# Optimization experiments

Measured on AMD Instinct MI355X. Metric: run time of the kernel, lower is better.

Reference implementation:

```python
import jax, jax.numpy as jnp
import numpy as np

N, C, OUT, S, NS = 8192, 256, 256, 8, 16  # points, in_planes, out_planes, share_planes, nsample
MID = OUT  # mid_planes = out_planes // 1
H = OUT // S  # linear_w bottleneck width
EPS = 1e-5


def _bn(x, g, b, m, v):
    # inference-mode BatchNorm1d over last (channel) dim
    return (x - m) * jax.lax.rsqrt(v + EPS) * g + b


def _knn_idx(p, k):
    # squared euclidean distances, (N,N); indices of k nearest (self included)
    sq = jnp.sum(p * p, axis=1)
    d = sq[:, None] + sq[None, :] - 2.0 * (p @ p.T)
    return jax.lax.top_k(-jax.lax.stop_gradient(d), k)[1]  # (N, k) int32


def setup_inputs() -> dict:
    key = jax.random.key(0)
    ks = jax.random.split(key, 24)
    g = lambda i, shape, s=0.05: jax.random.normal(ks[i], shape, jnp.float32) * s
    u = lambda i, shape: jax.random.uniform(ks[i], shape, dtype=jnp.float32)
    return {
        'p': u(0, (N, 3)),
        'x': g(1, (N, C), 1.0),
        'w_q': g(2, (C, MID)), 'b_q': jnp.zeros((MID,), jnp.float32),
        'w_k': g(3, (C, MID)), 'b_k': jnp.zeros((MID,), jnp.float32),
        'w_v': g(4, (C, OUT)), 'b_v': jnp.zeros((OUT,), jnp.float32),
        'p_w1': g(5, (3, 3), 0.5), 'p_b1': jnp.zeros((3,), jnp.float32),
        'p_bn_g': u(6, (3,)) + 0.5, 'p_bn_b': g(7, (3,), 0.1),
        'p_bn_m': g(8, (3,), 0.1), 'p_bn_v': u(9, (3,)) + 0.5,
        'p_w2': g(10, (3, OUT), 0.5), 'p_b2': jnp.zeros((OUT,), jnp.float32),
        'w_bn1_g': u(11, (MID,)) + 0.5, 'w_bn1_b': g(12, (MID,), 0.1),
        'w_bn1_m': g(13, (MID,), 0.1), 'w_bn1_v': u(14, (MID,)) + 0.5,
        'w_l1_w': g(15, (MID, H)), 'w_l1_b': jnp.zeros((H,), jnp.float32),
        'w_bn2_g': u(16, (H,)) + 0.5, 'w_bn2_b': g(17, (H,), 0.1),
        'w_bn2_m': g(18, (H,), 0.1), 'w_bn2_v': u(19, (H,)) + 0.5,
        'w_l2_w': g(20, (H, H)), 'w_l2_b': jnp.zeros((H,), jnp.float32),
    }


def reference(p, x, w_q, b_q, w_k, b_k, w_v, b_v,
              p_w1, p_b1, p_bn_g, p_bn_b, p_bn_m, p_bn_v, p_w2, p_b2,
              w_bn1_g, w_bn1_b, w_bn1_m, w_bn1_v, w_l1_w, w_l1_b,
              w_bn2_g, w_bn2_b, w_bn2_m, w_bn2_v, w_l2_w, w_l2_b):
    # PointTransformerLayer forward (single point cloud, o = [N])
    xq = x @ w_q + b_q            # (N, MID)
    xk = x @ w_k + b_k            # (N, MID)
    xv = x @ w_v + b_v            # (N, OUT)

    idx = _knn_idx(p, NS)         # (N, NS) KNN neighbor indices
    pr_xyz = p[idx] - p[:, None, :]   # (N, NS, 3) relative coords (with_xyz=True)
    xk_g = xk[idx]                # (N, NS, MID) gathered keys
    xv_g = xv[idx]                # (N, NS, OUT) gathered values

    # linear_p: Linear(3,3) -> BN -> ReLU -> Linear(3, OUT)
    pr = jax.nn.relu(_bn(pr_xyz @ p_w1 + p_b1, p_bn_g, p_bn_b, p_bn_m, p_bn_v))
    pr = pr @ p_w2 + p_b2         # (N, NS, OUT)

    # einops reduce 'n ns (i j)->n ns j' with j=MID is identity since MID==OUT
    r_qk = xk_g - xq[:, None, :] + pr   # (N, NS, MID)

    # linear_w: BN -> ReLU -> Linear(MID,H) -> BN -> ReLU -> Linear(H,H)
    w = jax.nn.relu(_bn(r_qk, w_bn1_g, w_bn1_b, w_bn1_m, w_bn1_v)) @ w_l1_w + w_l1_b
    w = jax.nn.relu(_bn(w, w_bn2_g, w_bn2_b, w_bn2_m, w_bn2_v)) @ w_l2_w + w_l2_b
    w = jax.nn.softmax(w, axis=1)       # softmax over neighbors (dim=1)

    v = (xv_g + pr).reshape(N, NS, S, H)      # 'n ns (s i) -> n ns s i'
    out = jnp.einsum('ntsi,nti->nsi', v, w)   # weighted aggregation over neighbors
    return out.reshape(N, OUT)
```

## Files before the change

### kernel.cpp

```cpp
#include <hip/hip_runtime.h>
#include <hip/hip_bf16.h>
#include <math.h>

#define N_PTS 8192
#define C_IN  256
#define OUT_C 256
#define NSAMP 16
#define H_W   32
#define EPSBN 1e-5f
#define GDIM  8
#define NCELL (GDIM * GDIM * GDIM)
#define CAPC  768

typedef short bf16x8 __attribute__((ext_vector_type(8)));
typedef float f32x4  __attribute__((ext_vector_type(4)));

__device__ __forceinline__ float dist2(const float4 a, const float4 b) {
  float dot = a.x * b.x + a.y * b.y + a.z * b.z;
  return a.w + b.w - 2.0f * dot;
}

__device__ __forceinline__ unsigned long long make_key(float d, int j) {
  unsigned int di = __float_as_uint(d);
  unsigned int ord = ((int)di >= 0) ? (di ^ 0x80000000u) : ~di;
  return ((unsigned long long)ord << 32) | (unsigned int)j;
}

__device__ __forceinline__ void chain_insert(unsigned long long (&ak)[16], unsigned long long key) {
  if (key < ak[0]) {
    #pragma unroll
    for (int s = 0; s < 15; ++s) {
      unsigned long long mn = ak[s] < key ? ak[s] : key;
      unsigned long long nx = ak[s + 1];
      ak[s] = nx > mn ? nx : mn;
    }
    ak[15] = ak[15] < key ? ak[15] : key;
  }
}

__device__ __forceinline__ void merge16(unsigned long long (&A)[16], int m) {
  unsigned long long B[16], t[16];
  #pragma unroll
  for (int s = 0; s < 16; ++s) B[s] = __shfl_xor(A[s], m, 64);
  #pragma unroll
  for (int s = 0; s < 16; ++s) t[s] = A[s] < B[15 - s] ? A[s] : B[15 - s];
  #pragma unroll
  for (int k = 8; k >= 1; k >>= 1) {
    #pragma unroll
    for (int s = 0; s < 16; ++s) {
      if (!(s & k)) {
        unsigned long long lo = t[s] < t[s | k] ? t[s] : t[s | k];
        unsigned long long hi = t[s] < t[s | k] ? t[s | k] : t[s];
        t[s] = lo; t[s | k] = hi;
      }
    }
  }
  #pragma unroll
  for (int s = 0; s < 16; ++s) A[s] = t[s];
}

__global__ __launch_bounds__(256) void prep_kernel(
    const float* __restrict__ p, const float* __restrict__ x,
    const float* __restrict__ wq, const float* __restrict__ wk, const float* __restrict__ wv,
    const float* __restrict__ bq, const float* __restrict__ bk, const float* __restrict__ bv,
    const float* __restrict__ l1w, const float* __restrict__ l2w,
    float4* __restrict__ p4, __hip_bfloat16* __restrict__ Bp, float* __restrict__ biasp,
    __hip_bfloat16* __restrict__ x_bf,
    __hip_bfloat16* __restrict__ l1wp, __hip_bfloat16* __restrict__ l2wp,
    int* __restrict__ hist, int* __restrict__ pt_cell) {
  int tid = blockIdx.x * blockDim.x + threadIdx.x;
  if (tid < 48 * 32 * 16 * 8) {
    int kj = tid & 7, n = (tid >> 3) & 15, kb = (tid >> 7) & 31, nt = tid >> 12;
    int k = kb * 8 + kj, col = nt * 16 + n;
    float v;
    if (col < 256)      v = wq[k * 256 + col];
    else if (col < 512) v = wk[k * 256 + (col - 256)];
    else                v = wv[k * 256 + (col - 512)];
    Bp[tid] = __float2bfloat16(v);
  }
  if (tid < 768) {
    biasp[tid] = tid < 256 ? bq[tid] : (tid < 512 ? bk[tid - 256] : bv[tid - 512]);
  }
  if (tid < 8192) {
    int kj = tid & 7, n = (tid >> 3) & 15, kb = (tid >> 7) & 31, nt = (tid >> 12) & 1;
    int k = kb * 8 + kj, col = nt * 16 + n;
    l1wp[tid] = __float2bfloat16(l1w[k * 32 + col]);
  }
  if (tid < 1024) {
    int kj = tid & 7, n = (tid >> 3) & 15, kb = (tid >> 7) & 3, nt = (tid >> 9) & 1;
    int k = kb * 8 + kj, col = nt * 16 + n;
    l2wp[tid] = __float2bfloat16(l2w[k * 32 + col]);
  }
  if (tid < N_PTS) {
    float px = p[tid * 3 + 0], py = p[tid * 3 + 1], pz = p[tid * 3 + 2];
    float sq = px * px;
    sq += py * py;
    sq += pz * pz;
    p4[tid] = make_float4(px, py, pz, sq);
    int cx = min(GDIM - 1, max(0, (int)(px * GDIM)));
    int cy = min(GDIM - 1, max(0, (int)(py * GDIM)));
    int cz = min(GDIM - 1, max(0, (int)(pz * GDIM)));
    int cell = (cz * GDIM + cy) * GDIM + cx;
    pt_cell[tid] = cell;
    atomicAdd(&hist[cell], 1);
  }
  if (tid < N_PTS * C_IN) x_bf[tid] = __float2bfloat16(x[tid]);
}

__global__ __launch_bounds__(512) void scan512(const int* __restrict__ hist, int* __restrict__ cell_start) {
  __shared__ int buf[NCELL];
  int t = threadIdx.x;
  buf[t] = hist[t];
  __syncthreads();
  for (int off = 1; off < NCELL; off <<= 1) {
    int add = (t >= off) ? buf[t - off] : 0;
    __syncthreads();
    buf[t] += add;
    __syncthreads();
  }
  cell_start[t + 1] = buf[t];
  if (t == 0) cell_start[0] = 0;
}

__global__ __launch_bounds__(256) void scatter_kernel(
    const float4* __restrict__ p4, const int* __restrict__ pt_cell,
    const int* __restrict__ cell_start, int* __restrict__ cursor,
    float4* __restrict__ sp4, int* __restrict__ sidx, int* __restrict__ rank) {
  int tid = blockIdx.x * blockDim.x + threadIdx.x;
  if (tid < N_PTS) {
    int c = pt_cell[tid];
    int pos = cell_start[c] + atomicAdd(&cursor[c], 1);
    sp4[pos] = p4[tid];
    sidx[pos] = tid;
    rank[tid] = pos;
  }
}

__global__ __launch_bounds__(256) void knn_grid(
    const float4* __restrict__ sp4, const int* __restrict__ sidx,
    const int* __restrict__ cell_start, int* __restrict__ nbr) {
  __shared__ float4 cpos[CAPC];
  __shared__ int    cidx[CAPC];
  __shared__ int cell_s0_s[27];
  __shared__ int pref_s[28];
  __shared__ int nc_s, total_s;

  const int cell = blockIdx.x;
  const int tid = threadIdx.x;
  const int hcx = cell & 7, hcy = (cell >> 3) & 7, hcz = cell >> 6;
  const int cs = cell_start[cell], ce = cell_start[cell + 1];

  const int ax0 = max(hcx - 1, 0), ax1 = min(hcx + 1, GDIM - 1);
  const int ay0 = max(hcy - 1, 0), ay1 = min(hcy + 1, GDIM - 1);
  const int az0 = max(hcz - 1, 0), az1 = min(hcz + 1, GDIM - 1);

  if (tid == 0) {
    int off = 0, m = 0;
    for (int cz = az0; cz <= az1; ++cz)
      for (int cy = ay0; cy <= ay1; ++cy)
        for (int cx = ax0; cx <= ax1; ++cx) {
          int cc = (cz * GDIM + cy) * GDIM + cx;
          cell_s0_s[m] = cell_start[cc];
          pref_s[m] = off;
          off += cell_start[cc + 1] - cell_start[cc];
          ++m;
        }
    pref_s[m] = off;
    nc_s = m;
    total_s = off;
  }
  __syncthreads();
  const int nc = nc_s, total = total_s;

  for (int idx = tid; idx < total && idx < CAPC; idx += 256) {
    int c = 0;
    while (c + 1 < nc && pref_s[c + 1] <= idx) ++c;
    int g = cell_s0_s[c] + (idx - pref_s[c]);
    cpos[idx] = sp4[g];
    cidx[idx] = sidx[g];
  }
  __syncthreads();

  const int ptl = tid >> 4, slice = tid & 15;

  for (int p0 = cs; p0 < ce; p0 += 16) {
    const int np = min(16, ce - p0);
    const bool pok = ptl < np;
    const int ld = pok ? (p0 + ptl) : cs;
    const float4 pi = sp4[ld];
    const int orig = sidx[ld];

    unsigned long long ak[16];
    #pragma unroll
    for (int s = 0; s < 16; ++s) ak[s] = ~0ULL;

    for (int idx = slice; idx < total; idx += 16) {
      float4 q;
      int qi;
      if (idx < CAPC) { q = cpos[idx]; qi = cidx[idx]; }
      else {
        int c = 0;
        while (c + 1 < nc && pref_s[c + 1] <= idx) ++c;
        int g = cell_s0_s[c] + (idx - pref_s[c]);
        q = sp4[g]; qi = sidx[g];
      }
      chain_insert(ak, make_key(dist2(pi, q), qi));
    }

    unsigned long long asc[16];
    #pragma unroll
    for (int s = 0; s < 16; ++s) asc[s] = ak[15 - s];
    merge16(asc, 1);
    merge16(asc, 2);
    merge16(asc, 4);
    merge16(asc, 8);

    if (slice == 0 && pok) {
      unsigned long long akm[16];
      #pragma unroll
      for (int s = 0; s < 16; ++s) akm[s] = asc[15 - s];
      float r;
      if (akm[0] == ~0ULL) {
        r = 1e9f;
      } else {
        unsigned int ord = (unsigned int)(akm[0] >> 32);
        unsigned int di = (ord & 0x80000000u) ? (ord ^ 0x80000000u) : ~ord;
        float d16 = __uint_as_float(di);
        r = sqrtf(fmaxf(d16, 0.f)) * 1.001f + 1e-4f;
      }
      int lx = (int)fminf(fmaxf(floorf((pi.x - r) * GDIM), 0.f), (float)(GDIM - 1));
      int ux = (int)fminf(fmaxf(floorf((pi.x + r) * GDIM), 0.f), (float)(GDIM - 1));
      int ly = (int)fminf(fmaxf(floorf((pi.y - r) * GDIM), 0.f), (float)(GDIM - 1));
      int uy = (int)fminf(fmaxf(floorf((pi.y + r) * GDIM), 0.f), (float)(GDIM - 1));
      int lz = (int)fminf(fmaxf(floorf((pi.z - r) * GDIM), 0.f), (float)(GDIM - 1));
      int uz = (int)fminf(fmaxf(floorf((pi.z + r) * GDIM), 0.f), (float)(GDIM - 1));
      if (lx < ax0 || ux > ax1 || ly < ay0 || uy > ay1 || lz < az0 || uz > az1) {
        for (int cz = lz; cz <= uz; ++cz)
          for (int cy = ly; cy <= uy; ++cy)
            for (int cx = lx; cx <= ux; ++cx) {
              if (cx >= ax0 && cx <= ax1 && cy >= ay0 && cy <= ay1 && cz >= az0 && cz <= az1)
                continue;
              int cc = (cz * GDIM + cy) * GDIM + cx;
              int s0 = cell_start[cc], e0 = cell_start[cc + 1];
              for (int k = s0; k < e0; ++k) {
                float4 q = sp4[k];
                chain_insert(akm, make_key(dist2(pi, q), sidx[k]));
              }
            }
      }
      #pragma unroll
      for (int s = 0; s < 16; ++s) nbr[orig * NSAMP + s] = (int)(akm[s] & 0xFFFFFFFFu);
    }
  }
}

__global__ __launch_bounds__(256) void gemm_qkv_mfma(
    const __hip_bfloat16* __restrict__ x_bf, const __hip_bfloat16* __restrict__ Bp,
    const float* __restrict__ biasp, const int* __restrict__ rank,
    __hip_bfloat16* __restrict__ xqkv) {
  const int w = threadIdx.x >> 6;
  const int lane = threadIdx.x & 63;
  const int gw = blockIdx.x * 4 + w;
  const int m0 = (gw & 127) * 64;
  const int nt4 = (gw >> 7) * 4;
  const int n = lane & 15, q = lane >> 4;

  f32x4 acc[4][4];
  #pragma unroll
  for (int mi = 0; mi < 4; ++mi)
    #pragma unroll
    for (int ni = 0; ni < 4; ++ni) acc[mi][ni] = (f32x4){0.f, 0.f, 0.f, 0.f};

  for (int k0 = 0; k0 < 256; k0 += 32) {
    bf16x8 af[4], bfr[4];
    #pragma unroll
    for (int mi = 0; mi < 4; ++mi)
      af[mi] = *(const bf16x8*)&x_bf[(size_t)(m0 + mi * 16 + n) * 256 + k0 + q * 8];
    #pragma unroll
    for (int ni = 0; ni < 4; ++ni)
      bfr[ni] = *(const bf16x8*)&Bp[(size_t)(nt4 + ni) * 4096 + (k0 >> 3) * 128 + q * 128 + n * 8];
    #pragma unroll
    for (int mi = 0; mi < 4; ++mi)
      #pragma unroll
      for (int ni = 0; ni < 4; ++ni)
        acc[mi][ni] = __builtin_amdgcn_mfma_f32_16x16x32_bf16(af[mi], bfr[ni], acc[mi][ni], 0, 0, 0);
  }
  float bcol[4];
  #pragma unroll
  for (int ni = 0; ni < 4; ++ni) bcol[ni] = biasp[(nt4 + ni) * 16 + n];
  #pragma unroll
  for (int mi = 0; mi < 4; ++mi)
    #pragma unroll
    for (int r = 0; r < 4; ++r) {
      int row = m0 + mi * 16 + q * 4 + r;
      size_t srow = (size_t)rank[row];
      #pragma unroll
      for (int ni = 0; ni < 4; ++ni)
        xqkv[srow * 768 + (nt4 + ni) * 16 + n] = __float2bfloat16(acc[mi][ni][r] + bcol[ni]);
    }
}

__global__ __launch_bounds__(256) void fused_pt(
    const float4* __restrict__ sp4, const int* __restrict__ sidx, const int* __restrict__ rank,
    const __hip_bfloat16* __restrict__ xqkv, const int* __restrict__ nbr,
    const float* __restrict__ pw1, const float* __restrict__ pb1,
    const float* __restrict__ pbng, const float* __restrict__ pbnb,
    const float* __restrict__ pbnm, const float* __restrict__ pbnv,
    const float* __restrict__ pw2, const float* __restrict__ pb2,
    const float* __restrict__ bn1g, const float* __restrict__ bn1b,
    const float* __restrict__ bn1m, const float* __restrict__ bn1v,
    const __hip_bfloat16* __restrict__ l1wp, const float* __restrict__ l1b,
    const float* __restrict__ bn2g, const float* __restrict__ bn2b,
    const float* __restrict__ bn2m, const float* __restrict__ bn2v,
    const __hip_bfloat16* __restrict__ l2wp, const float* __restrict__ l2b,
    float* __restrict__ out) {
  __shared__ __align__(16) __hip_bfloat16 a_s[NSAMP][264];
  __shared__ __align__(16) __hip_bfloat16 h1_s[NSAMP][40];
  __shared__ float w_s[NSAMP][33];
  __shared__ float q3_s[NSAMP][4];
  __shared__ int jn[NSAMP];

  const int b = blockIdx.x;
  const int i = sidx[b];
  const int tid = threadIdx.x;

  if (tid < NSAMP) {
    int j = nbr[i * NSAMP + tid];
    int k = rank[j];
    jn[tid] = k;
    float4 pj = sp4[k];
    float4 pc = sp4[b];
    float rx = pj.x - pc.x;
    float ry = pj.y - pc.y;
    float rz = pj.z - pc.z;
    #pragma unroll
    for (int c3 = 0; c3 < 3; ++c3) {
      float t = rx * pw1[0 * 3 + c3] + ry * pw1[1 * 3 + c3] + rz * pw1[2 * 3 + c3] + pb1[c3];
      t = (t - pbnm[c3]) * rsqrtf(pbnv[c3] + EPSBN) * pbng[c3] + pbnb[c3];
      q3_s[tid][c3] = fmaxf(t, 0.f);
    }
  }
  __syncthreads();

  const int c = tid;
  const float xq_c = __bfloat162float(xqkv[(size_t)b * 768 + c]);
  const float s1 = bn1g[c] * rsqrtf(bn1v[c] + EPSBN);
  const float o1 = bn1b[c] - bn1m[c] * s1;
  const float w2c0 = pw2[c], w2c1 = pw2[256 + c], w2c2 = pw2[512 + c];
  const float pb2c = pb2[c];
  #pragma unroll
  for (int t = 0; t < NSAMP; ++t) {
    int k = jn[t];
    float prv = q3_s[t][0] * w2c0 + q3_s[t][1] * w2c1 + q3_s[t][2] * w2c2 + pb2c;
    float xkv = __bfloat162float(xqkv[(size_t)k * 768 + 256 + c]);
    float r = xkv - xq_c + prv;
    a_s[t][c] = __float2bfloat16(fmaxf(r * s1 + o1, 0.f));
  }
  __syncthreads();

  const int wv_ = tid >> 6;
  const int lane = tid & 63;
  const int nn = lane & 15, q = lane >> 4;
  if (wv_ < 2) {
    f32x4 acc = {0.f, 0.f, 0.f, 0.f};
    #pragma unroll
    for (int k0 = 0; k0 < 256; k0 += 32) {
      bf16x8 a = *(const bf16x8*)&a_s[nn][k0 + q * 8];
      bf16x8 bb = *(const bf16x8*)&l1wp[wv_ * 4096 + (k0 >> 3) * 128 + q * 128 + nn * 8];
      acc = __builtin_amdgcn_mfma_f32_16x16x32_bf16(a, bb, acc, 0, 0, 0);
    }
    int h = wv_ * 16 + nn;
    float s2 = bn2g[h] * rsqrtf(bn2v[h] + EPSBN);
    float o2 = bn2b[h] - bn2m[h] * s2;
    float l1bh = l1b[h];
    #pragma unroll
    for (int r = 0; r < 4; ++r)
      h1_s[q * 4 + r][h] = __float2bfloat16(fmaxf((acc[r] + l1bh) * s2 + o2, 0.f));
  }
  __syncthreads();

  if (wv_ < 2) {
    bf16x8 a = *(const bf16x8*)&h1_s[nn][q * 8];
    bf16x8 bb = *(const bf16x8*)&l2wp[wv_ * 512 + q * 128 + nn * 8];
    f32x4 z = {0.f, 0.f, 0.f, 0.f};
    f32x4 d = __builtin_amdgcn_mfma_f32_16x16x32_bf16(a, bb, z, 0, 0, 0);
    int h = wv_ * 16 + nn;
    float l2bh = l2b[h];
    #pragma unroll
    for (int r = 0; r < 4; ++r) w_s[q * 4 + r][h] = d[r] + l2bh;
  }
  __syncthreads();

  if (tid < H_W) {
    int h = tid;
    float m = -1e30f;
    #pragma unroll
    for (int t = 0; t < NSAMP; ++t) m = fmaxf(m, w_s[t][h]);
    float e[NSAMP];
    float ssum = 0.f;
    #pragma unroll
    for (int t = 0; t < NSAMP; ++t) { e[t] = __expf(w_s[t][h] - m); ssum += e[t]; }
    float inv = 1.f / ssum;
    #pragma unroll
    for (int t = 0; t < NSAMP; ++t) w_s[t][h] = e[t] * inv;
  }
  __syncthreads();

  const int h = c & 31;
  float acc6 = 0.f;
  #pragma unroll
  for (int t = 0; t < NSAMP; ++t) {
    int k = jn[t];
    float xv = __bfloat162float(xqkv[(size_t)k * 768 + 512 + c]);
    float prv = q3_s[t][0] * w2c0 + q3_s[t][1] * w2c1 + q3_s[t][2] * w2c2 + pb2c;
    acc6 += (xv + prv) * w_s[t][h];
  }
  out[(size_t)i * OUT_C + c] = acc6;
}

extern "C" void kernel_launch(void* const* d_in, const int* in_sizes, int n_in,
                              void* d_out, int out_size, void* d_ws, size_t ws_size,
                              hipStream_t stream) {
  const float* p    = (const float*)d_in[0];
  const float* x    = (const float*)d_in[1];
  const float* wq   = (const float*)d_in[2];
  const float* bq   = (const float*)d_in[3];
  const float* wk   = (const float*)d_in[4];
  const float* bk   = (const float*)d_in[5];
  const float* wv   = (const float*)d_in[6];
  const float* bv   = (const float*)d_in[7];
  const float* pw1  = (const float*)d_in[8];
  const float* pb1  = (const float*)d_in[9];
  const float* pbng = (const float*)d_in[10];
  const float* pbnb = (const float*)d_in[11];
  const float* pbnm = (const float*)d_in[12];
  const float* pbnv = (const float*)d_in[13];
  const float* pw2  = (const float*)d_in[14];
  const float* pb2  = (const float*)d_in[15];
  const float* bn1g = (const float*)d_in[16];
  const float* bn1b = (const float*)d_in[17];
  const float* bn1m = (const float*)d_in[18];
  const float* bn1v = (const float*)d_in[19];
  const float* l1w  = (const float*)d_in[20];
  const float* l1b  = (const float*)d_in[21];
  const float* bn2g = (const float*)d_in[22];
  const float* bn2b = (const float*)d_in[23];
  const float* bn2m = (const float*)d_in[24];
  const float* bn2v = (const float*)d_in[25];
  const float* l2w  = (const float*)d_in[26];
  const float* l2b  = (const float*)d_in[27];
  float* out = (float*)d_out;

  char* ws = (char*)d_ws;
  float4* p4       = (float4*)(ws + 0x000000);
  float*  biasp    = (float*)(ws + 0x040000);
  int*    hist     = (int*)(ws + 0x042000);
  int*    cursor   = (int*)(ws + 0x042800);
  int*    cell_st  = (int*)(ws + 0x043000);
  int*    pt_cell  = (int*)(ws + 0x044000);
  float4* sp4      = (float4*)(ws + 0x050000);
  int*    sidx     = (int*)(ws + 0x070000);
  __hip_bfloat16* l1wp = (__hip_bfloat16*)(ws + 0x080000);
  __hip_bfloat16* l2wp = (__hip_bfloat16*)(ws + 0x084000);
  int*    rank     = (int*)(ws + 0x088000);
  int*    nbr      = (int*)(ws + 0x090000);
  __hip_bfloat16* Bp   = (__hip_bfloat16*)(ws + 0x110000);
  __hip_bfloat16* x_bf = (__hip_bfloat16*)(ws + 0x170000);
  __hip_bfloat16* xqkv = (__hip_bfloat16*)(ws + 0x570000);

  hipMemsetAsync(ws + 0x042000, 0, 0x1000, stream);
  prep_kernel<<<dim3(N_PTS), dim3(256), 0, stream>>>(
      p, x, wq, wk, wv, bq, bk, bv, l1w, l2w, p4, Bp, biasp, x_bf, l1wp, l2wp,
      hist, pt_cell);
  scan512<<<dim3(1), dim3(NCELL), 0, stream>>>(hist, cell_st);
  scatter_kernel<<<dim3(32), dim3(256), 0, stream>>>(p4, pt_cell, cell_st, cursor, sp4, sidx, rank);
  gemm_qkv_mfma<<<dim3(384), dim3(256), 0, stream>>>(x_bf, Bp, biasp, rank, xqkv);
  knn_grid<<<dim3(NCELL), dim3(256), 0, stream>>>(sp4, sidx, cell_st, nbr);
  fused_pt<<<dim3(N_PTS), dim3(256), 0, stream>>>(
      sp4, sidx, rank, xqkv, nbr, pw1, pb1, pbng, pbnb, pbnm, pbnv, pw2, pb2,
      bn1g, bn1b, bn1m, bn1v, l1wp, l1b, bn2g, bn2b, bn2m, bn2v, l2wp, l2b, out);
}
```

Before: 221.8 us.

## Use radius-filtered candidate sets with rank selection for KNN; permute x before GEMM

KNN no longer keeps a 16-entry sorted chain per slice followed by a shuffle merge network. Each point now collects candidates inside a density-estimated radius into shared memory and picks the 16 nearest by counting ranks. If too few or too many candidates fall inside the radius, one lane falls back to a serial full scan. Separately, x is gathered into sorted-point order during the bf16 conversion, so the GEMM writes rows contiguously instead of scattering through rank. The radius heuristic depends on the point distribution, and the serial fallback plus the extra block-wide syncs could be slow on uneven inputs.

Result: slower. 321.8 us (+45.1%).

```diff
diff --git a/kernel.cpp b/kernel.cpp
--- a/kernel.cpp
+++ b/kernel.cpp
@@ -11,6 +11,7 @@
 #define GDIM  8
 #define NCELL (GDIM * GDIM * GDIM)
 #define CAPC  768
+#define CAP_H 56
 
 typedef short bf16x8 __attribute__((ext_vector_type(8)));
 typedef float f32x4  __attribute__((ext_vector_type(4)));
@@ -38,34 +39,12 @@
   }
 }
 
-__device__ __forceinline__ void merge16(unsigned long long (&A)[16], int m) {
-  unsigned long long B[16], t[16];
-  #pragma unroll
-  for (int s = 0; s < 16; ++s) B[s] = __shfl_xor(A[s], m, 64);
-  #pragma unroll
-  for (int s = 0; s < 16; ++s) t[s] = A[s] < B[15 - s] ? A[s] : B[15 - s];
-  #pragma unroll
-  for (int k = 8; k >= 1; k >>= 1) {
-    #pragma unroll
-    for (int s = 0; s < 16; ++s) {
-      if (!(s & k)) {
-        unsigned long long lo = t[s] < t[s | k] ? t[s] : t[s | k];
-        unsigned long long hi = t[s] < t[s | k] ? t[s | k] : t[s];
-        t[s] = lo; t[s | k] = hi;
-      }
-    }
-  }
-  #pragma unroll
-  for (int s = 0; s < 16; ++s) A[s] = t[s];
-}
-
 __global__ __launch_bounds__(256) void prep_kernel(
-    const float* __restrict__ p, const float* __restrict__ x,
+    const float* __restrict__ p,
     const float* __restrict__ wq, const float* __restrict__ wk, const float* __restrict__ wv,
     const float* __restrict__ bq, const float* __restrict__ bk, const float* __restrict__ bv,
     const float* __restrict__ l1w, const float* __restrict__ l2w,
     float4* __restrict__ p4, __hip_bfloat16* __restrict__ Bp, float* __restrict__ biasp,
-    __hip_bfloat16* __restrict__ x_bf,
     __hip_bfloat16* __restrict__ l1wp, __hip_bfloat16* __restrict__ l2wp,
     int* __restrict__ hist, int* __restrict__ pt_cell) {
   int tid = blockIdx.x * blockDim.x + threadIdx.x;
@@ -104,7 +83,6 @@
     pt_cell[tid] = cell;
     atomicAdd(&hist[cell], 1);
   }
-  if (tid < N_PTS * C_IN) x_bf[tid] = __float2bfloat16(x[tid]);
 }
 
 __global__ __launch_bounds__(512) void scan512(const int* __restrict__ hist, int* __restrict__ cell_start) {
@@ -136,14 +114,26 @@
   }
 }
 
+__global__ __launch_bounds__(256) void xbf_kernel(
+    const float* __restrict__ x, const int* __restrict__ sidx,
+    __hip_bfloat16* __restrict__ x_bf) {
+  const int b = blockIdx.x;
+  const int c = threadIdx.x;
+  x_bf[(size_t)b * C_IN + c] = __float2bfloat16(x[(size_t)sidx[b] * C_IN + c]);
+}
+
 __global__ __launch_bounds__(256) void knn_grid(
     const float4* __restrict__ sp4, const int* __restrict__ sidx,
     const int* __restrict__ cell_start, int* __restrict__ nbr) {
   __shared__ float4 cpos[CAPC];
   __shared__ int    cidx[CAPC];
+  __shared__ unsigned long long hk_s[16][CAP_H];
+  __shared__ unsigned long long okey_s[16][16];
+  __shared__ int cnt_s[16];
   __shared__ int cell_s0_s[27];
   __shared__ int pref_s[28];
   __shared__ int nc_s, total_s;
+  __shared__ float r2_s;
 
   const int cell = blockIdx.x;
   const int tid = threadIdx.x;
@@ -168,9 +158,15 @@
     pref_s[m] = off;
     nc_s = m;
     total_s = off;
+    int nbc = (ax1 - ax0 + 1) * (ay1 - ay0 + 1) * (az1 - az0 + 1);
+    float vol = (float)nbc / 512.0f;
+    float rho = (float)off / vol;
+    float r = 1.30f * cbrtf(3.8197186f / rho);
+    r2_s = r * r;
   }
   __syncthreads();
   const int nc = nc_s, total = total_s;
+  const float r2 = r2_s;
 
   for (int idx = tid; idx < total && idx < CAPC; idx += 256) {
     int c = 0;
@@ -190,35 +186,63 @@
     const float4 pi = sp4[ld];
     const int orig = sidx[ld];
 
-    unsigned long long ak[16];
-    #pragma unroll
-    for (int s = 0; s < 16; ++s) ak[s] = ~0ULL;
-
-    for (int idx = slice; idx < total; idx += 16) {
-      float4 q;
-      int qi;
-      if (idx < CAPC) { q = cpos[idx]; qi = cidx[idx]; }
-      else {
-        int c = 0;
-        while (c + 1 < nc && pref_s[c + 1] <= idx) ++c;
-        int g = cell_s0_s[c] + (idx - pref_s[c]);
-        q = sp4[g]; qi = sidx[g];
+    if (tid < 16) cnt_s[tid] = 0;
+    __syncthreads();
+
+    if (pok) {
+      for (int idx = slice; idx < total; idx += 16) {
+        float4 q;
+        int qi;
+        if (idx < CAPC) { q = cpos[idx]; qi = cidx[idx]; }
+        else {
+          int c = 0;
+          while (c + 1 < nc && pref_s[c + 1] <= idx) ++c;
+          int g = cell_s0_s[c] + (idx - pref_s[c]);
+          q = sp4[g]; qi = sidx[g];
+        }
+        float d = dist2(pi, q);
+        if (d <= r2) {
+          int pos = atomicAdd(&cnt_s[ptl], 1);
+          if (pos < CAP_H) hk_s[ptl][pos] = make_key(d, qi);
+        }
       }
-      chain_insert(ak, make_key(dist2(pi, q), qi));
     }
-
-    unsigned long long asc[16];
-    #pragma unroll
-    for (int s = 0; s < 16; ++s) asc[s] = ak[15 - s];
-    merge16(asc, 1);
-    merge16(asc, 2);
-    merge16(asc, 4);
-    merge16(asc, 8);
+    __syncthreads();
+
+    const int cnt = cnt_s[ptl];
+    const bool fb = (cnt < 16) || (cnt > CAP_H);
+
+    if (pok && !fb) {
+      for (int i = slice; i < cnt; i += 16) {
+        unsigned long long key = hk_s[ptl][i];
+        int rk = 0;
+        for (int j = 0; j < cnt; ++j) rk += (hk_s[ptl][j] < key) ? 1 : 0;
+        if (rk < 16) okey_s[ptl][rk] = key;
+      }
+    }
+    __syncthreads();
 
     if (slice == 0 && pok) {
       unsigned long long akm[16];
-      #pragma unroll
-      for (int s = 0; s < 16; ++s) akm[s] = asc[15 - s];
+      if (!fb) {
+        #pragma unroll
+        for (int s = 0; s < 16; ++s) akm[s] = okey_s[ptl][15 - s];
+      } else {
+        #pragma unroll
+        for (int s = 0; s < 16; ++s) akm[s] = ~0ULL;
+        for (int idx = 0; idx < total; ++idx) {
+          float4 q;
+          int qi;
+          if (idx < CAPC) { q = cpos[idx]; qi = cidx[idx]; }
+          else {
+            int c = 0;
+            while (c + 1 < nc && pref_s[c + 1] <= idx) ++c;
+            int g = cell_s0_s[c] + (idx - pref_s[c]);
+            q = sp4[g]; qi = sidx[g];
+          }
+          chain_insert(akm, make_key(dist2(pi, q), qi));
+        }
+      }
       float r;
       if (akm[0] == ~0ULL) {
         r = 1e9f;
@@ -251,13 +275,13 @@
       #pragma unroll
       for (int s = 0; s < 16; ++s) nbr[orig * NSAMP + s] = (int)(akm[s] & 0xFFFFFFFFu);
     }
+    __syncthreads();
   }
 }
 
 __global__ __launch_bounds__(256) void gemm_qkv_mfma(
     const __hip_bfloat16* __restrict__ x_bf, const __hip_bfloat16* __restrict__ Bp,
-    const float* __restrict__ biasp, const int* __restrict__ rank,
-    __hip_bfloat16* __restrict__ xqkv) {
+    const float* __restrict__ biasp, __hip_bfloat16* __restrict__ xqkv) {
   const int w = threadIdx.x >> 6;
   const int lane = threadIdx.x & 63;
   const int gw = blockIdx.x * 4 + w;
@@ -285,19 +309,16 @@
       for (int ni = 0; ni < 4; ++ni)
         acc[mi][ni] = __builtin_amdgcn_mfma_f32_16x16x32_bf16(af[mi], bfr[ni], acc[mi][ni], 0, 0, 0);
   }
-  float bcol[4];
   #pragma unroll
-  for (int ni = 0; ni < 4; ++ni) bcol[ni] = biasp[(nt4 + ni) * 16 + n];
-  #pragma unroll
-  for (int mi = 0; mi < 4; ++mi)
-    #pragma unroll
-    for (int r = 0; r < 4; ++r) {
-      int row = m0 + mi * 16 + q * 4 + r;
-      size_t srow = (size_t)rank[row];
+  for (int ni = 0; ni < 4; ++ni) {
+    int col = (nt4 + ni) * 16 + n;
+    float b = biasp[col];
+    #pragma unroll
+    for (int mi = 0; mi < 4; ++mi)
       #pragma unroll
-      for (int ni = 0; ni < 4; ++ni)
-        xqkv[srow * 768 + (nt4 + ni) * 16 + n] = __float2bfloat16(acc[mi][ni][r] + bcol[ni]);
-    }
+      for (int r = 0; r < 4; ++r)
+        xqkv[(size_t)(m0 + mi * 16 + q * 4 + r) * 768 + col] = __float2bfloat16(acc[mi][ni][r] + b);
+  }
 }
 
 __global__ __launch_bounds__(256) void fused_pt(
@@ -469,12 +490,13 @@
   __hip_bfloat16* xqkv = (__hip_bfloat16*)(ws + 0x570000);
 
   hipMemsetAsync(ws + 0x042000, 0, 0x1000, stream);
-  prep_kernel<<<dim3(N_PTS), dim3(256), 0, stream>>>(
-      p, x, wq, wk, wv, bq, bk, bv, l1w, l2w, p4, Bp, biasp, x_bf, l1wp, l2wp,
+  prep_kernel<<<dim3(768), dim3(256), 0, stream>>>(
+      p, wq, wk, wv, bq, bk, bv, l1w, l2w, p4, Bp, biasp, l1wp, l2wp,
       hist, pt_cell);
   scan512<<<dim3(1), dim3(NCELL), 0, stream>>>(hist, cell_st);
   scatter_kernel<<<dim3(32), dim3(256), 0, stream>>>(p4, pt_cell, cell_st, cursor, sp4, sidx, rank);
-  gemm_qkv_mfma<<<dim3(384), dim3(256), 0, stream>>>(x_bf, Bp, biasp, rank, xqkv);
+  xbf_kernel<<<dim3(N_PTS), dim3(256), 0, stream>>>(x, sidx, x_bf);
+  gemm_qkv_mfma<<<dim3(384), dim3(256), 0, stream>>>(x_bf, Bp, biasp, xqkv);
   knn_grid<<<dim3(NCELL), dim3(256), 0, stream>>>(sp4, sidx, cell_st, nbr);
   fused_pt<<<dim3(N_PTS), dim3(256), 0, stream>>>(
       sp4, sidx, rank, xqkv, nbr, pw1, pb1, pbng, pbnb, pbnm, pbnv, pw2, pb2,
```
